# Performance work log

Measured on AMD Instinct MI355X. Metric: run time of the kernel, lower is better.

The kernel has to match this reference:

```python
import jax, jax.numpy as jnp
import numpy as np

K = 128
HEADS = 8
B = 4
T = 2048


def setup_inputs() -> dict:
    key = jax.random.key(0)
    ks = jax.random.split(key, 6)
    x = jax.random.normal(ks[0], (B, T, K), dtype=jnp.float32)
    s = 1.0 / np.sqrt(K)
    # torch nn.Linear weights are (out_features, in_features)
    Wq = jax.random.uniform(ks[1], (HEADS * K, K), dtype=jnp.float32, minval=-s, maxval=s)
    Wk = jax.random.uniform(ks[2], (HEADS * K, K), dtype=jnp.float32, minval=-s, maxval=s)
    Wv = jax.random.uniform(ks[3], (HEADS * K, K), dtype=jnp.float32, minval=-s, maxval=s)
    su = 1.0 / np.sqrt(HEADS * K)
    Wu = jax.random.uniform(ks[4], (K, HEADS * K), dtype=jnp.float32, minval=-su, maxval=su)
    bu = jax.random.uniform(ks[5], (K,), dtype=jnp.float32, minval=-su, maxval=su)
    return {"x": x, "Wq": Wq, "Wk": Wk, "Wv": Wv, "Wu": Wu, "bu": bu}


def reference(x, Wq, Wk, Wv, Wu, bu):
    b, t, k = x.shape
    h = HEADS
    # project: Linear(k, k*h) then view(b,t,h,k); weight reshaped to (h, k_out, k_in)
    q = jnp.einsum('btk,hdk->bhtd', x, Wq.reshape(h, k, k))
    kk = jnp.einsum('btk,hdk->bhtd', x, Wk.reshape(h, k, k))
    v = jnp.einsum('btk,hdk->bhtd', x, Wv.reshape(h, k, k))
    scale = jnp.asarray(k, x.dtype) ** 0.25
    q = q / scale
    kk = kk / scale
    dot = jnp.einsum('bhtd,bhsd->bhts', q, kk)  # [b,h,t,t]
    att = jax.nn.softmax(dot, axis=-1)
    out = jnp.einsum('bhts,bhsd->bhtd', att, v)  # [b,h,t,k]
    out = out.transpose(0, 2, 1, 3).reshape(b, t, h * k)
    return out @ Wu.T + bu
```

## Files before the change

### kernel.cpp

```cpp
#include <hip/hip_runtime.h>
#include <cmath>

namespace {

constexpr int HEADS = 8;
constexpr int Bn = 4;
constexpr int Tn = 2048;
constexpr int Dn = 128;
constexpr float Q_PRESCALE = 0.1275174340f;

typedef _Float16 half8 __attribute__((ext_vector_type(8)));
typedef _Float16 half4 __attribute__((ext_vector_type(4)));
typedef float f32x4 __attribute__((ext_vector_type(4)));

__global__ __launch_bounds__(256) void cast_kernel(
    const float* __restrict__ x, const float* __restrict__ Wq, const float* __restrict__ Wk,
    const float* __restrict__ Wv, const float* __restrict__ Wu, _Float16* __restrict__ xh,
    _Float16* __restrict__ WH) {
  const int idx = blockIdx.x * 256 + threadIdx.x;
  const size_t base = (size_t)idx * 8;
  const float* src;
  _Float16* dst;
  if (base < 1048576) {
    src = x + base;
    dst = xh + base;
  } else {
    const size_t r = base - 1048576;
    const int s = (int)(r >> 17);
    src = ((s == 0) ? Wq : (s == 1) ? Wk : (s == 2) ? Wv : Wu) + (r & 131071);
    dst = WH + r;
  }
  const float4 a = *reinterpret_cast<const float4*>(src);
  const float4 b = *reinterpret_cast<const float4*>(src + 4);
  half8 h;
  h[0] = (_Float16)a.x; h[1] = (_Float16)a.y; h[2] = (_Float16)a.z; h[3] = (_Float16)a.w;
  h[4] = (_Float16)b.x; h[5] = (_Float16)b.y; h[6] = (_Float16)b.z; h[7] = (_Float16)b.w;
  *reinterpret_cast<half8*>(dst) = h;
}

__global__ __launch_bounds__(256, 4) void proj_kernel(const _Float16* __restrict__ xh,
                                                      const _Float16* __restrict__ WH,
                                                      _Float16* __restrict__ Qh,
                                                      _Float16* __restrict__ Kh,
                                                      _Float16* __restrict__ Vt) {
  __shared__ _Float16 sB[128 * 136];
  const int tid = threadIdx.x;
  const int w = tid >> 6, lane = tid & 63, quad = lane >> 4, l16 = lane & 15;
  const int m0 = blockIdx.x * 128;
  const int n0 = blockIdx.y * 128;

#pragma unroll
  for (int it = 0; it < 8; ++it) {
    const int fid = tid + it * 256;
    const int r = fid >> 4, g = fid & 15;
    const half8 v = *reinterpret_cast<const half8*>(WH + (size_t)(n0 + r) * 128 + g * 8);
    const int p = g ^ (r & 15);
    *reinterpret_cast<half8*>(sB + r * 128 + p * 8) = v;
  }

  half8 af[2][4];
  const _Float16* xp = xh + (size_t)(m0 + w * 32 + l16) * 128 + quad * 8;
#pragma unroll
  for (int mt = 0; mt < 2; ++mt)
#pragma unroll
    for (int kk = 0; kk < 4; ++kk)
      af[mt][kk] = *reinterpret_cast<const half8*>(xp + mt * 16 * 128 + kk * 32);

  __syncthreads();

  f32x4 acc[2][8];
#pragma unroll
  for (int mt = 0; mt < 2; ++mt)
#pragma unroll
    for (int nt = 0; nt < 8; ++nt) acc[mt][nt] = (f32x4){0.f, 0.f, 0.f, 0.f};

#pragma unroll
  for (int kk = 0; kk < 4; ++kk)
#pragma unroll
    for (int nt = 0; nt < 8; ++nt) {
      const int r = nt * 16 + l16;
      const int p = (kk * 4 + quad) ^ l16;
      const half8 bf = *reinterpret_cast<const half8*>(sB + r * 128 + p * 8);
      acc[0][nt] = __builtin_amdgcn_mfma_f32_16x16x32_f16(af[0][kk], bf, acc[0][nt], 0, 0, 0);
      acc[1][nt] = __builtin_amdgcn_mfma_f32_16x16x32_f16(af[1][kk], bf, acc[1][nt], 0, 0, 0);
    }

  const int sel = n0 >> 10;
  const int h = (n0 >> 7) & 7;
  const int b = m0 >> 11;
  const int t0b = m0 & 2047;
  const int bh = b * HEADS + h;
  const float scale = (sel == 0) ? Q_PRESCALE : 1.0f;

  __syncthreads();

  if (sel < 2) {
#pragma unroll
    for (int mt = 0; mt < 2; ++mt)
#pragma unroll
      for (int nt = 0; nt < 8; ++nt)
#pragma unroll
        for (int r = 0; r < 4; ++r)
          sB[(w * 32 + mt * 16 + quad * 4 + r) * 136 + nt * 16 + l16] =
              (_Float16)(acc[mt][nt][r] * scale);
  } else {
#pragma unroll
    for (int mt = 0; mt < 2; ++mt)
#pragma unroll
      for (int nt = 0; nt < 8; ++nt)
#pragma unroll
        for (int r = 0; r < 4; ++r)
          sB[(nt * 16 + l16) * 136 + w * 32 + mt * 16 + quad * 4 + r] = (_Float16)acc[mt][nt][r];
  }
  __syncthreads();

  _Float16* dstbase;
  size_t rstride;
  if (sel == 0) {
    dstbase = Qh + ((size_t)bh * Tn + t0b) * Dn;
    rstride = Dn;
  } else if (sel == 1) {
    dstbase = Kh + ((size_t)bh * Tn + t0b) * Dn;
    rstride = Dn;
  } else {
    dstbase = Vt + ((size_t)bh * Dn) * Tn + t0b;
    rstride = Tn;
  }
#pragma unroll
  for (int it = 0; it < 8; ++it) {
    const int fid = tid + it * 256;
    const int r = fid >> 4, g = fid & 15;
    const half8 v = *reinterpret_cast<const half8*>(sB + r * 136 + g * 8);
    *reinterpret_cast<half8*>(dstbase + (size_t)r * rstride + g * 8) = v;
  }
}

__global__ __launch_bounds__(256, 2) void flash_kernel(const _Float16* __restrict__ Qh,
                                                       const _Float16* __restrict__ Kh,
                                                       const _Float16* __restrict__ Vt,
                                                       _Float16* __restrict__ Obh) {
  __shared__ _Float16 sK[64 * 128];
  __shared__ _Float16 sV[128 * 64];
  __shared__ _Float16 sP[4][32 * 64];
  __shared__ float sL[4][2][16];

  const int tid = threadIdx.x;
  const int w = tid >> 6;
  const int lane = tid & 63;
  const int quad = lane >> 4;
  const int l16 = lane & 15;
  const int qt = blockIdx.x;
  const int bh = blockIdx.y;

  half8 qf[2][4];
#pragma unroll
  for (int qg = 0; qg < 2; ++qg) {
    const _Float16* Qp =
        Qh + ((size_t)bh * Tn + qt * 128 + w * 32 + qg * 16 + l16) * Dn + quad * 8;
#pragma unroll
    for (int kk = 0; kk < 4; ++kk) qf[qg][kk] = *reinterpret_cast<const half8*>(Qp + kk * 32);
  }

  const _Float16* Kp = Kh + (size_t)bh * Tn * Dn;
  const _Float16* Vp = Vt + (size_t)bh * Dn * Tn;
  _Float16* sPw = sP[w];

  f32x4 o[2][8];
#pragma unroll
  for (int qg = 0; qg < 2; ++qg)
#pragma unroll
    for (int nt = 0; nt < 8; ++nt) o[qg][nt] = (f32x4){0.f, 0.f, 0.f, 0.f};
  float lsum[2] = {0.f, 0.f};

  half8 kreg[4], vreg[4];
  const int kr = tid >> 4, kg = tid & 15;
  const int vr = tid >> 3, vg = tid & 7;
#pragma unroll
  for (int it = 0; it < 4; ++it) {
    kreg[it] = *reinterpret_cast<const half8*>(Kp + (size_t)(kr + it * 16) * Dn + kg * 8);
    vreg[it] = *reinterpret_cast<const half8*>(Vp + (size_t)(vr + it * 32) * Tn + vg * 8);
  }

  for (int st = 0; st < Tn / 64; ++st) {
    __syncthreads();
#pragma unroll
    for (int it = 0; it < 4; ++it) {
      const int r = kr + it * 16;
      const int p = kg ^ (r & 15);
      *reinterpret_cast<half8*>(sK + r * 128 + p * 8) = kreg[it];
      const int rv = vr + it * 32;
      const int pv = vg ^ ((rv & 7) ^ ((rv >> 1) & 4));
      *reinterpret_cast<half8*>(sV + rv * 64 + pv * 8) = vreg[it];
    }
    if (st + 1 < Tn / 64) {
      const _Float16* knext = Kp + (size_t)(st + 1) * 64 * Dn;
      const _Float16* vnext = Vp + (st + 1) * 64;
#pragma unroll
      for (int it = 0; it < 4; ++it) {
        kreg[it] = *reinterpret_cast<const half8*>(knext + (size_t)(kr + it * 16) * Dn + kg * 8);
        vreg[it] = *reinterpret_cast<const half8*>(vnext + (size_t)(vr + it * 32) * Tn + vg * 8);
      }
    }
    __syncthreads();

    f32x4 s_t[2][4];
#pragma unroll
    for (int qg = 0; qg < 2; ++qg)
#pragma unroll
      for (int j = 0; j < 4; ++j) s_t[qg][j] = (f32x4){0.f, 0.f, 0.f, 0.f};
#pragma unroll
    for (int kk = 0; kk < 4; ++kk)
#pragma unroll
      for (int j = 0; j < 4; ++j) {
        const int p = (kk * 4 + quad) ^ l16;
        const half8 kf = *reinterpret_cast<const half8*>(sK + (j * 16 + l16) * 128 + p * 8);
        s_t[0][j] = __builtin_amdgcn_mfma_f32_16x16x32_f16(kf, qf[0][kk], s_t[0][j], 0, 0, 0);
        s_t[1][j] = __builtin_amdgcn_mfma_f32_16x16x32_f16(kf, qf[1][kk], s_t[1][j], 0, 0, 0);
      }

#pragma unroll
    for (int qg = 0; qg < 2; ++qg)
#pragma unroll
      for (int j = 0; j < 4; ++j) {
        f32x4 e;
        e[0] = __builtin_amdgcn_exp2f(s_t[qg][j][0]);
        e[1] = __builtin_amdgcn_exp2f(s_t[qg][j][1]);
        e[2] = __builtin_amdgcn_exp2f(s_t[qg][j][2]);
        e[3] = __builtin_amdgcn_exp2f(s_t[qg][j][3]);
        lsum[qg] += (e[0] + e[1]) + (e[2] + e[3]);
        half4 h4;
        h4[0] = (_Float16)e[0]; h4[1] = (_Float16)e[1];
        h4[2] = (_Float16)e[2]; h4[3] = (_Float16)e[3];
        const int g = j * 2 + (quad >> 1);
        const int p = g ^ (l16 & 7);
        *reinterpret_cast<half4*>(sPw + (qg * 16 + l16) * 64 + p * 8 + (quad & 1) * 4) = h4;
      }

#pragma unroll
    for (int kk2 = 0; kk2 < 2; ++kk2) {
      half8 pf[2];
#pragma unroll
      for (int qg = 0; qg < 2; ++qg) {
        const int pA = (kk2 * 4 + quad) ^ (l16 & 7);
        pf[qg] = *reinterpret_cast<const half8*>(sPw + (qg * 16 + l16) * 64 + pA * 8);
      }
#pragma unroll
      for (int nt = 0; nt < 8; ++nt) {
        const int r = nt * 16 + l16;
        const int pV = (kk2 * 4 + quad) ^ ((r & 7) ^ ((r >> 1) & 4));
        const half8 vf = *reinterpret_cast<const half8*>(sV + r * 64 + pV * 8);
        o[0][nt] = __builtin_amdgcn_mfma_f32_16x16x32_f16(pf[0], vf, o[0][nt], 0, 0, 0);
        o[1][nt] = __builtin_amdgcn_mfma_f32_16x16x32_f16(pf[1], vf, o[1][nt], 0, 0, 0);
      }
    }
  }

#pragma unroll
  for (int qg = 0; qg < 2; ++qg) {
    float ls = lsum[qg];
    ls += __shfl_xor(ls, 16);
    ls += __shfl_xor(ls, 32);
    if (quad == 0) sL[w][qg][l16] = 1.0f / ls;
  }
  const int b = bh >> 3, h = bh & 7;
#pragma unroll
  for (int qg = 0; qg < 2; ++qg) {
    const f32x4 inv4 = *reinterpret_cast<const f32x4*>(&sL[w][qg][quad * 4]);
#pragma unroll
    for (int r = 0; r < 4; ++r) {
      const size_t trow =
          (size_t)(b * Tn + qt * 128 + w * 32 + qg * 16 + quad * 4 + r) * (HEADS * Dn);
#pragma unroll
      for (int nt = 0; nt < 8; ++nt)
        Obh[trow + h * Dn + nt * 16 + l16] = (_Float16)(o[qg][nt][r] * inv4[r]);
    }
  }
}

__global__ __launch_bounds__(256, 4) void outproj_kernel(const _Float16* __restrict__ Obh,
                                                         const _Float16* __restrict__ Wuh,
                                                         const float* __restrict__ bu,
                                                         float* __restrict__ out) {
  __shared__ float sR[4 * 32 * 128];
  const int tid = threadIdx.x;
  const int w = tid >> 6, lane = tid & 63, quad = lane >> 4, l16 = lane & 15;
  const int r0 = blockIdx.x * 32;

  f32x4 acc[2][8];
#pragma unroll
  for (int mt = 0; mt < 2; ++mt)
#pragma unroll
    for (int nt = 0; nt < 8; ++nt) acc[mt][nt] = (f32x4){0.f, 0.f, 0.f, 0.f};

  const _Float16* ap = Obh + (size_t)(r0 + l16) * 1024 + w * 256 + quad * 8;
  const _Float16* bp = Wuh + (size_t)l16 * 1024 + w * 256 + quad * 8;

#pragma unroll
  for (int kk = 0; kk < 8; ++kk) {
    const half8 a0 = *reinterpret_cast<const half8*>(ap + kk * 32);
    const half8 a1 = *reinterpret_cast<const half8*>(ap + 16 * 1024 + kk * 32);
#pragma unroll
    for (int nt = 0; nt < 8; ++nt) {
      const half8 bf = *reinterpret_cast<const half8*>(bp + (size_t)nt * 16 * 1024 + kk * 32);
      acc[0][nt] = __builtin_amdgcn_mfma_f32_16x16x32_f16(a0, bf, acc[0][nt], 0, 0, 0);
      acc[1][nt] = __builtin_amdgcn_mfma_f32_16x16x32_f16(a1, bf, acc[1][nt], 0, 0, 0);
    }
  }

#pragma unroll
  for (int mt = 0; mt < 2; ++mt)
#pragma unroll
    for (int nt = 0; nt < 8; ++nt)
#pragma unroll
      for (int r = 0; r < 4; ++r)
        sR[w * 4096 + (mt * 16 + quad * 4 + r) * 128 + nt * 16 + l16] = acc[mt][nt][r];
  __syncthreads();

#pragma unroll
  for (int it = 0; it < 16; ++it) {
    const int idx = tid + it * 256;
    const int row = idx >> 7, col = idx & 127;
    const float v = sR[idx] + sR[4096 + idx] + sR[8192 + idx] + sR[12288 + idx] + bu[col];
    out[(size_t)(r0 + row) * Dn + col] = v;
  }
}

}

extern "C" void kernel_launch(void* const* d_in, const int* in_sizes, int n_in, void* d_out,
                              int out_size, void* d_ws, size_t ws_size, hipStream_t stream) {
  (void)in_sizes; (void)n_in; (void)out_size; (void)ws_size;
  const float* x = (const float*)d_in[0];
  const float* Wq = (const float*)d_in[1];
  const float* Wk = (const float*)d_in[2];
  const float* Wv = (const float*)d_in[3];
  const float* Wu = (const float*)d_in[4];
  const float* bu = (const float*)d_in[5];
  float* out = (float*)d_out;

  constexpr size_t NE = (size_t)Bn * HEADS * Tn * Dn;
  char* ws = (char*)d_ws;
  _Float16* xh = (_Float16*)ws;
  _Float16* WH = (_Float16*)(ws + 2097152);
  _Float16* Qh = (_Float16*)(ws + 4194304);
  _Float16* Kh = (_Float16*)(ws + 4194304 + NE * 2);
  _Float16* Vt = (_Float16*)(ws + 4194304 + NE * 4);
  _Float16* Obh = (_Float16*)(ws + 4194304 + NE * 6);
  _Float16* Wuh = WH + 393216;

  cast_kernel<<<dim3(768), 256, 0, stream>>>(x, Wq, Wk, Wv, Wu, xh, WH);
  proj_kernel<<<dim3(64, 24), 256, 0, stream>>>(xh, WH, Qh, Kh, Vt);
  flash_kernel<<<dim3(16, 32), 256, 0, stream>>>(Qh, Kh, Vt, Obh);
  outproj_kernel<<<dim3(256), 256, 0, stream>>>(Obh, Wuh, bu, out);
}
```

Measured before the change: 176.3 us.

## Load V fragments directly from global into registers, dropping shared V tile

Removes the shared-memory staging of V in the flash attention kernel. Each wave now reads its MFMA V operands directly from global memory (via L2/L1) into 16 half8 registers at the start of each key tile. This removes the LDS writes and reads for V and some LDS footprint. The cost is four-fold redundant global traffic across waves, a high register count that may hurt occupancy, and global load latency that is no longer prefetched a tile ahead. A syncthreads is also added before the final sL reads.

```diff
diff --git a/kernel.cpp b/kernel.cpp
--- a/kernel.cpp
+++ b/kernel.cpp
@@ -140,7 +140,6 @@
                                                        const _Float16* __restrict__ Vt,
                                                        _Float16* __restrict__ Obh) {
   __shared__ _Float16 sK[64 * 128];
-  __shared__ _Float16 sV[128 * 64];
   __shared__ _Float16 sP[4][32 * 64];
   __shared__ float sL[4][2][16];
 
@@ -162,7 +161,7 @@
   }
 
   const _Float16* Kp = Kh + (size_t)bh * Tn * Dn;
-  const _Float16* Vp = Vt + (size_t)bh * Dn * Tn;
+  const _Float16* Vl = Vt + (size_t)bh * Dn * Tn + (size_t)l16 * Tn + quad * 8;
   _Float16* sPw = sP[w];
 
   f32x4 o[2][8];
@@ -172,34 +171,33 @@
     for (int nt = 0; nt < 8; ++nt) o[qg][nt] = (f32x4){0.f, 0.f, 0.f, 0.f};
   float lsum[2] = {0.f, 0.f};
 
-  half8 kreg[4], vreg[4];
+  half8 kreg[4];
   const int kr = tid >> 4, kg = tid & 15;
-  const int vr = tid >> 3, vg = tid & 7;
-#pragma unroll
-  for (int it = 0; it < 4; ++it) {
+#pragma unroll
+  for (int it = 0; it < 4; ++it)
     kreg[it] = *reinterpret_cast<const half8*>(Kp + (size_t)(kr + it * 16) * Dn + kg * 8);
-    vreg[it] = *reinterpret_cast<const half8*>(Vp + (size_t)(vr + it * 32) * Tn + vg * 8);
-  }
 
   for (int st = 0; st < Tn / 64; ++st) {
+    half8 vfr[16];
+#pragma unroll
+    for (int kk2 = 0; kk2 < 2; ++kk2)
+#pragma unroll
+      for (int nt = 0; nt < 8; ++nt)
+        vfr[kk2 * 8 + nt] = *reinterpret_cast<const half8*>(
+            Vl + (size_t)(nt * 16) * Tn + st * 64 + kk2 * 32);
+
     __syncthreads();
 #pragma unroll
     for (int it = 0; it < 4; ++it) {
       const int r = kr + it * 16;
       const int p = kg ^ (r & 15);
       *reinterpret_cast<half8*>(sK + r * 128 + p * 8) = kreg[it];
-      const int rv = vr + it * 32;
-      const int pv = vg ^ ((rv & 7) ^ ((rv >> 1) & 4));
-      *reinterpret_cast<half8*>(sV + rv * 64 + pv * 8) = vreg[it];
     }
     if (st + 1 < Tn / 64) {
       const _Float16* knext = Kp + (size_t)(st + 1) * 64 * Dn;
-      const _Float16* vnext = Vp + (st + 1) * 64;
-#pragma unroll
-      for (int it = 0; it < 4; ++it) {
+#pragma unroll
+      for (int it = 0; it < 4; ++it)
         kreg[it] = *reinterpret_cast<const half8*>(knext + (size_t)(kr + it * 16) * Dn + kg * 8);
-        vreg[it] = *reinterpret_cast<const half8*>(vnext + (size_t)(vr + it * 32) * Tn + vg * 8);
-      }
     }
     __syncthreads();
 
@@ -246,9 +244,7 @@
       }
 #pragma unroll
       for (int nt = 0; nt < 8; ++nt) {
-        const int r = nt * 16 + l16;
-        const int pV = (kk2 * 4 + quad) ^ ((r & 7) ^ ((r >> 1) & 4));
-        const half8 vf = *reinterpret_cast<const half8*>(sV + r * 64 + pV * 8);
+        const half8 vf = vfr[kk2 * 8 + nt];
         o[0][nt] = __builtin_amdgcn_mfma_f32_16x16x32_f16(pf[0], vf, o[0][nt], 0, 0, 0);
         o[1][nt] = __builtin_amdgcn_mfma_f32_16x16x32_f16(pf[1], vf, o[1][nt], 0, 0, 0);
       }
@@ -262,6 +258,7 @@
     ls += __shfl_xor(ls, 32);
     if (quad == 0) sL[w][qg][l16] = 1.0f / ls;
   }
+  __syncthreads();
   const int b = bh >> 3, h = bh & 7;
 #pragma unroll
   for (int qg = 0; qg < 2; ++qg) {
```

New measurement: 223.3 us. 26.6% more time.

## Load K fragments directly from global into registers, bypassing shared memory

Applied to the files above, without the earlier changes.

Each warp now loads the full 64x128 K tile straight from global memory into 16 half8 MFMA operand registers instead of staging it cooperatively in shared memory. The next tile's K prefetch moves to just after the QK^T MFMAs. This removes the LDS writes and reads for K and halves shared memory use, which could allow more occupancy. In exchange, each of the 4 warps reads the same K tile from global/L2 (4x redundant traffic), register pressure rises by 64 VGPRs, and a syncthreads is added before the final normalization read.

```diff
diff --git a/kernel.cpp b/kernel.cpp
--- a/kernel.cpp
+++ b/kernel.cpp
@@ -139,7 +139,6 @@
                                                        const _Float16* __restrict__ Kh,
                                                        const _Float16* __restrict__ Vt,
                                                        _Float16* __restrict__ Obh) {
-  __shared__ _Float16 sK[64 * 128];
   __shared__ _Float16 sV[128 * 64];
   __shared__ _Float16 sP[4][32 * 64];
   __shared__ float sL[4][2][16];
@@ -161,7 +160,7 @@
     for (int kk = 0; kk < 4; ++kk) qf[qg][kk] = *reinterpret_cast<const half8*>(Qp + kk * 32);
   }
 
-  const _Float16* Kp = Kh + (size_t)bh * Tn * Dn;
+  const _Float16* Kl = Kh + ((size_t)bh * Tn + l16) * Dn + quad * 8;
   const _Float16* Vp = Vt + (size_t)bh * Dn * Tn;
   _Float16* sPw = sP[w];
 
@@ -172,35 +171,27 @@
     for (int nt = 0; nt < 8; ++nt) o[qg][nt] = (f32x4){0.f, 0.f, 0.f, 0.f};
   float lsum[2] = {0.f, 0.f};
 
-  half8 kreg[4], vreg[4];
-  const int kr = tid >> 4, kg = tid & 15;
+  half8 kfr[16];
+#pragma unroll
+  for (int kk = 0; kk < 4; ++kk)
+#pragma unroll
+    for (int j = 0; j < 4; ++j)
+      kfr[kk * 4 + j] = *reinterpret_cast<const half8*>(Kl + (size_t)(j * 16) * Dn + kk * 32);
+
+  half8 vreg[4];
   const int vr = tid >> 3, vg = tid & 7;
 #pragma unroll
-  for (int it = 0; it < 4; ++it) {
-    kreg[it] = *reinterpret_cast<const half8*>(Kp + (size_t)(kr + it * 16) * Dn + kg * 8);
+  for (int it = 0; it < 4; ++it)
     vreg[it] = *reinterpret_cast<const half8*>(Vp + (size_t)(vr + it * 32) * Tn + vg * 8);
-  }
 
   for (int st = 0; st < Tn / 64; ++st) {
     __syncthreads();
 #pragma unroll
     for (int it = 0; it < 4; ++it) {
-      const int r = kr + it * 16;
-      const int p = kg ^ (r & 15);
-      *reinterpret_cast<half8*>(sK + r * 128 + p * 8) = kreg[it];
       const int rv = vr + it * 32;
       const int pv = vg ^ ((rv & 7) ^ ((rv >> 1) & 4));
       *reinterpret_cast<half8*>(sV + rv * 64 + pv * 8) = vreg[it];
     }
-    if (st + 1 < Tn / 64) {
-      const _Float16* knext = Kp + (size_t)(st + 1) * 64 * Dn;
-      const _Float16* vnext = Vp + (st + 1) * 64;
-#pragma unroll
-      for (int it = 0; it < 4; ++it) {
-        kreg[it] = *reinterpret_cast<const half8*>(knext + (size_t)(kr + it * 16) * Dn + kg * 8);
-        vreg[it] = *reinterpret_cast<const half8*>(vnext + (size_t)(vr + it * 32) * Tn + vg * 8);
-      }
-    }
     __syncthreads();
 
     f32x4 s_t[2][4];
@@ -212,11 +203,23 @@
     for (int kk = 0; kk < 4; ++kk)
 #pragma unroll
       for (int j = 0; j < 4; ++j) {
-        const int p = (kk * 4 + quad) ^ l16;
-        const half8 kf = *reinterpret_cast<const half8*>(sK + (j * 16 + l16) * 128 + p * 8);
+        const half8 kf = kfr[kk * 4 + j];
         s_t[0][j] = __builtin_amdgcn_mfma_f32_16x16x32_f16(kf, qf[0][kk], s_t[0][j], 0, 0, 0);
         s_t[1][j] = __builtin_amdgcn_mfma_f32_16x16x32_f16(kf, qf[1][kk], s_t[1][j], 0, 0, 0);
       }
+
+    if (st + 1 < Tn / 64) {
+      const _Float16* Kn = Kl + (size_t)(st + 1) * 64 * Dn;
+#pragma unroll
+      for (int kk = 0; kk < 4; ++kk)
+#pragma unroll
+        for (int j = 0; j < 4; ++j)
+          kfr[kk * 4 + j] = *reinterpret_cast<const half8*>(Kn + (size_t)(j * 16) * Dn + kk * 32);
+      const _Float16* Vn = Vp + (st + 1) * 64;
+#pragma unroll
+      for (int it = 0; it < 4; ++it)
+        vreg[it] = *reinterpret_cast<const half8*>(Vn + (size_t)(vr + it * 32) * Tn + vg * 8);
+    }
 
 #pragma unroll
     for (int qg = 0; qg < 2; ++qg)
@@ -262,6 +265,7 @@
     ls += __shfl_xor(ls, 32);
     if (quad == 0) sL[w][qg][l16] = 1.0f / ls;
   }
+  __syncthreads();
   const int b = bh >> 3, h = bh & 7;
 #pragma unroll
   for (int qg = 0; qg < 2; ++qg) {
```

Result: slower. 226.9 us (+28.7%).

## Fuse fp32-to-fp16 casts into projection kernels and shrink outproj tile

Applied to the files above, without the earlier changes.

Removes the separate cast kernel and converts x and the weights from fp32 to fp16 on the fly inside proj_kernel and outproj_kernel. This cuts one launch and the round trip of the fp16 copies through memory. The output projection now handles 16 rows per block over twice as many blocks, which halves its shared memory and accumulators. A __syncthreads is also added before the final normalization read in the flash kernel. In exchange, each weight element is re-read as fp32 and converted again by every block that uses it, so weight traffic goes up.

```diff
diff --git a/kernel.cpp b/kernel.cpp
--- a/kernel.cpp
+++ b/kernel.cpp
@@ -13,33 +13,19 @@
 typedef _Float16 half4 __attribute__((ext_vector_type(4)));
 typedef float f32x4 __attribute__((ext_vector_type(4)));
 
-__global__ __launch_bounds__(256) void cast_kernel(
-    const float* __restrict__ x, const float* __restrict__ Wq, const float* __restrict__ Wk,
-    const float* __restrict__ Wv, const float* __restrict__ Wu, _Float16* __restrict__ xh,
-    _Float16* __restrict__ WH) {
-  const int idx = blockIdx.x * 256 + threadIdx.x;
-  const size_t base = (size_t)idx * 8;
-  const float* src;
-  _Float16* dst;
-  if (base < 1048576) {
-    src = x + base;
-    dst = xh + base;
-  } else {
-    const size_t r = base - 1048576;
-    const int s = (int)(r >> 17);
-    src = ((s == 0) ? Wq : (s == 1) ? Wk : (s == 2) ? Wv : Wu) + (r & 131071);
-    dst = WH + r;
-  }
+__device__ __forceinline__ half8 cvt8(const float* src) {
   const float4 a = *reinterpret_cast<const float4*>(src);
   const float4 b = *reinterpret_cast<const float4*>(src + 4);
   half8 h;
   h[0] = (_Float16)a.x; h[1] = (_Float16)a.y; h[2] = (_Float16)a.z; h[3] = (_Float16)a.w;
   h[4] = (_Float16)b.x; h[5] = (_Float16)b.y; h[6] = (_Float16)b.z; h[7] = (_Float16)b.w;
-  *reinterpret_cast<half8*>(dst) = h;
-}
-
-__global__ __launch_bounds__(256, 4) void proj_kernel(const _Float16* __restrict__ xh,
-                                                      const _Float16* __restrict__ WH,
+  return h;
+}
+
+__global__ __launch_bounds__(256, 4) void proj_kernel(const float* __restrict__ x,
+                                                      const float* __restrict__ Wq,
+                                                      const float* __restrict__ Wk,
+                                                      const float* __restrict__ Wv,
                                                       _Float16* __restrict__ Qh,
                                                       _Float16* __restrict__ Kh,
                                                       _Float16* __restrict__ Vt) {
@@ -48,23 +34,26 @@
   const int w = tid >> 6, lane = tid & 63, quad = lane >> 4, l16 = lane & 15;
   const int m0 = blockIdx.x * 128;
   const int n0 = blockIdx.y * 128;
+  const int sel = n0 >> 10;
+  const float* W = (sel == 0) ? Wq : (sel == 1) ? Wk : Wv;
+  const int nw = n0 & 1023;
 
 #pragma unroll
   for (int it = 0; it < 8; ++it) {
     const int fid = tid + it * 256;
     const int r = fid >> 4, g = fid & 15;
-    const half8 v = *reinterpret_cast<const half8*>(WH + (size_t)(n0 + r) * 128 + g * 8);
+    const half8 v = cvt8(W + (size_t)(nw + r) * 128 + g * 8);
     const int p = g ^ (r & 15);
     *reinterpret_cast<half8*>(sB + r * 128 + p * 8) = v;
   }
 
   half8 af[2][4];
-  const _Float16* xp = xh + (size_t)(m0 + w * 32 + l16) * 128 + quad * 8;
+  const float* xp = x + (size_t)(m0 + w * 32 + l16) * 128 + quad * 8;
 #pragma unroll
   for (int mt = 0; mt < 2; ++mt)
 #pragma unroll
     for (int kk = 0; kk < 4; ++kk)
-      af[mt][kk] = *reinterpret_cast<const half8*>(xp + mt * 16 * 128 + kk * 32);
+      af[mt][kk] = cvt8(xp + mt * 16 * 128 + kk * 32);
 
   __syncthreads();
 
@@ -85,7 +74,6 @@
       acc[1][nt] = __builtin_amdgcn_mfma_f32_16x16x32_f16(af[1][kk], bf, acc[1][nt], 0, 0, 0);
     }
 
-  const int sel = n0 >> 10;
   const int h = (n0 >> 7) & 7;
   const int b = m0 >> 11;
   const int t0b = m0 & 2047;
@@ -262,6 +250,7 @@
     ls += __shfl_xor(ls, 32);
     if (quad == 0) sL[w][qg][l16] = 1.0f / ls;
   }
+  __syncthreads();
   const int b = bh >> 3, h = bh & 7;
 #pragma unroll
   for (int qg = 0; qg < 2; ++qg) {
@@ -278,49 +267,43 @@
 }
 
 __global__ __launch_bounds__(256, 4) void outproj_kernel(const _Float16* __restrict__ Obh,
-                                                         const _Float16* __restrict__ Wuh,
+                                                         const float* __restrict__ Wu,
                                                          const float* __restrict__ bu,
                                                          float* __restrict__ out) {
-  __shared__ float sR[4 * 32 * 128];
+  __shared__ float sR[4 * 16 * 128];
   const int tid = threadIdx.x;
   const int w = tid >> 6, lane = tid & 63, quad = lane >> 4, l16 = lane & 15;
-  const int r0 = blockIdx.x * 32;
-
-  f32x4 acc[2][8];
-#pragma unroll
-  for (int mt = 0; mt < 2; ++mt)
-#pragma unroll
-    for (int nt = 0; nt < 8; ++nt) acc[mt][nt] = (f32x4){0.f, 0.f, 0.f, 0.f};
+  const int r0 = blockIdx.x * 16;
+
+  f32x4 acc[8];
+#pragma unroll
+  for (int nt = 0; nt < 8; ++nt) acc[nt] = (f32x4){0.f, 0.f, 0.f, 0.f};
 
   const _Float16* ap = Obh + (size_t)(r0 + l16) * 1024 + w * 256 + quad * 8;
-  const _Float16* bp = Wuh + (size_t)l16 * 1024 + w * 256 + quad * 8;
+  const float* bp = Wu + (size_t)l16 * 1024 + w * 256 + quad * 8;
 
 #pragma unroll
   for (int kk = 0; kk < 8; ++kk) {
     const half8 a0 = *reinterpret_cast<const half8*>(ap + kk * 32);
-    const half8 a1 = *reinterpret_cast<const half8*>(ap + 16 * 1024 + kk * 32);
 #pragma unroll
     for (int nt = 0; nt < 8; ++nt) {
-      const half8 bf = *reinterpret_cast<const half8*>(bp + (size_t)nt * 16 * 1024 + kk * 32);
-      acc[0][nt] = __builtin_amdgcn_mfma_f32_16x16x32_f16(a0, bf, acc[0][nt], 0, 0, 0);
-      acc[1][nt] = __builtin_amdgcn_mfma_f32_16x16x32_f16(a1, bf, acc[1][nt], 0, 0, 0);
-    }
-  }
-
-#pragma unroll
-  for (int mt = 0; mt < 2; ++mt)
-#pragma unroll
-    for (int nt = 0; nt < 8; ++nt)
-#pragma unroll
-      for (int r = 0; r < 4; ++r)
-        sR[w * 4096 + (mt * 16 + quad * 4 + r) * 128 + nt * 16 + l16] = acc[mt][nt][r];
-  __syncthreads();
-
-#pragma unroll
-  for (int it = 0; it < 16; ++it) {
+      const half8 bf = cvt8(bp + (size_t)nt * 16 * 1024 + kk * 32);
+      acc[nt] = __builtin_amdgcn_mfma_f32_16x16x32_f16(a0, bf, acc[nt], 0, 0, 0);
+    }
+  }
+
+#pragma unroll
+  for (int nt = 0; nt < 8; ++nt)
+#pragma unroll
+    for (int r = 0; r < 4; ++r)
+      sR[w * 2048 + (quad * 4 + r) * 128 + nt * 16 + l16] = acc[nt][r];
+  __syncthreads();
+
+#pragma unroll
+  for (int it = 0; it < 8; ++it) {
     const int idx = tid + it * 256;
     const int row = idx >> 7, col = idx & 127;
-    const float v = sR[idx] + sR[4096 + idx] + sR[8192 + idx] + sR[12288 + idx] + bu[col];
+    const float v = sR[idx] + sR[2048 + idx] + sR[4096 + idx] + sR[6144 + idx] + bu[col];
     out[(size_t)(r0 + row) * Dn + col] = v;
   }
 }
@@ -340,16 +323,12 @@
 
   constexpr size_t NE = (size_t)Bn * HEADS * Tn * Dn;
   char* ws = (char*)d_ws;
-  _Float16* xh = (_Float16*)ws;
-  _Float16* WH = (_Float16*)(ws + 2097152);
-  _Float16* Qh = (_Float16*)(ws + 4194304);
-  _Float16* Kh = (_Float16*)(ws + 4194304 + NE * 2);
-  _Float16* Vt = (_Float16*)(ws + 4194304 + NE * 4);
-  _Float16* Obh = (_Float16*)(ws + 4194304 + NE * 6);
-  _Float16* Wuh = WH + 393216;
-
-  cast_kernel<<<dim3(768), 256, 0, stream>>>(x, Wq, Wk, Wv, Wu, xh, WH);
-  proj_kernel<<<dim3(64, 24), 256, 0, stream>>>(xh, WH, Qh, Kh, Vt);
+  _Float16* Qh = (_Float16*)ws;
+  _Float16* Kh = (_Float16*)(ws + NE * 2);
+  _Float16* Vt = (_Float16*)(ws + NE * 4);
+  _Float16* Obh = (_Float16*)(ws + NE * 6);
+
+  proj_kernel<<<dim3(64, 24), 256, 0, stream>>>(x, Wq, Wk, Wv, Qh, Kh, Vt);
   flash_kernel<<<dim3(16, 32), 256, 0, stream>>>(Qh, Kh, Vt, Obh);
-  outproj_kernel<<<dim3(256), 256, 0, stream>>>(Obh, Wuh, bu, out);
-}
+  outproj_kernel<<<dim3(512), 256, 0, stream>>>(Obh, Wu, bu, out);
+}
```

Result: slower. 198.1 us (+12.4%).
